# Performance work log

Measured on AMD Instinct MI355X. Metric: run time of the kernel, lower is better.

## Reference

```python
import jax, jax.numpy as jnp
import numpy as np

D_MODEL = 1024
NUM_HEADS = 16


def setup_inputs() -> dict:
    key = jax.random.key(0)
    k1, k2, k3, k4, k5 = jax.random.split(key, 5)
    b, n, d = 4, 2048, D_MODEL
    s = 1.0 / np.sqrt(d)
    x = jax.random.normal(k1, (b, n, d), dtype=jnp.float32)
    v_w = jax.random.uniform(k2, (d, d), dtype=jnp.float32, minval=-s, maxval=s)  # Linear weight [out,in]
    v_b = jax.random.uniform(k3, (d,), dtype=jnp.float32, minval=-s, maxval=s)
    o_w = jax.random.uniform(k4, (d, d), dtype=jnp.float32, minval=-s, maxval=s)
    o_b = jax.random.uniform(k5, (d,), dtype=jnp.float32, minval=-s, maxval=s)
    return {"x": x, "v_w": v_w, "v_b": v_b, "o_w": o_w, "o_b": o_b}


def reference(x, v_w, v_b, o_w, o_b):
    b, n, d = x.shape
    h = NUM_HEADS
    dh = d // h
    # shared QKV projection: q = k = v
    v = jnp.einsum('bnd,ed->bne', x, v_w) + v_b            # [b,n,d]
    v = v.reshape(b, n, h, dh).transpose(0, 2, 1, 3)        # [b,h,n,dh]
    scale = 1.0 / jnp.sqrt(jnp.asarray(dh, dtype=x.dtype))
    scores = jnp.einsum('bhnd,bhmd->bhnm', v, v) * scale    # [b,h,n,n]
    attn = jax.nn.softmax(scores, axis=-1)
    out = jnp.einsum('bhnm,bhmd->bhnd', attn, v)            # [b,h,n,dh]
    out = out.transpose(0, 2, 1, 3).reshape(b, n, d)        # concat heads
    return jnp.einsum('bnd,ed->bne', out, o_w) + o_b
```

## Files before the change

### kernel.cpp

```cpp
#include <hip/hip_runtime.h>
#include <stdint.h>

typedef __attribute__((ext_vector_type(8))) short short8;
typedef __attribute__((ext_vector_type(4))) float f32x4;
typedef __attribute__((ext_vector_type(4))) unsigned int u32x4;
typedef __attribute__((ext_vector_type(2))) unsigned int u32x2;

#define MFMA16(a, b, c) __builtin_amdgcn_mfma_f32_16x16x32_bf16((a), (b), (c), 0, 0, 0)

#define GLD_LDS16(g, l)                                                                  \
    __builtin_amdgcn_global_load_lds((const __attribute__((address_space(1))) void*)(g), \
                                     (__attribute__((address_space(3))) void*)(l), 16, 0, 0)

#if defined(__has_builtin)
#if __has_builtin(__builtin_amdgcn_exp2f)
#define FAST_EXP2(x) __builtin_amdgcn_exp2f(x)
#endif
#endif
#ifndef FAST_EXP2
__device__ __forceinline__ float fast_exp2_asm(float x) {
    float r;
    asm volatile("v_exp_f32 %0, %1\ns_nop 1" : "=v"(r) : "v"(x));
    return r;
}
#define FAST_EXP2(x) fast_exp2_asm(x)
#endif

__device__ __forceinline__ float bf2f(unsigned short u) {
    unsigned int x = ((unsigned int)u) << 16;
    float f;
    __builtin_memcpy(&f, &x, 4);
    return f;
}
__device__ __forceinline__ unsigned short f2bf(float f) {
    unsigned int x;
    __builtin_memcpy(&x, &f, 4);
    unsigned int r = x + 0x7FFFu + ((x >> 16) & 1u);
    return (unsigned short)(r >> 16);
}
__device__ __forceinline__ unsigned int pack2bf(float a, float b) {
    unsigned int ua, ub;
    __builtin_memcpy(&ua, &a, 4);
    __builtin_memcpy(&ub, &b, 4);
    return __builtin_amdgcn_perm(ub + 0x8000u, ua + 0x8000u, 0x07060302u);
}
__device__ __forceinline__ u32x4 cvt8(const float* p) {
    f32x4 g0 = *(const f32x4*)p;
    f32x4 g1 = *(const f32x4*)(p + 4);
    u32x4 r;
    r.x = pack2bf(g0[0], g0[1]);
    r.y = pack2bf(g0[2], g0[3]);
    r.z = pack2bf(g1[0], g1[1]);
    r.w = pack2bf(g1[2], g1[3]);
    return r;
}

__global__ __launch_bounds__(256) void cvt_kernel(const float* __restrict__ in,
                                                  unsigned short* __restrict__ out, int n8) {
    int i = blockIdx.x * 256 + threadIdx.x;
    if (i < n8) *(u32x4*)(out + (size_t)i * 8) = cvt8(in + (size_t)i * 8);
}

template <int MODE>
__global__ __launch_bounds__(256) void gemm_dma_kernel(
    const unsigned short* __restrict__ A, const unsigned short* __restrict__ B,
    const float* __restrict__ bias, void* __restrict__ Cv, int M, int N, int K) {
    __shared__ __align__(16) unsigned short As[2][2][128 * 32];
    __shared__ __align__(16) unsigned short Bs[2][2][128 * 32];

    const int tid = threadIdx.x;
    const int wave = tid >> 6, lane = tid & 63;
    const int l15 = lane & 15, quad = lane >> 4;
    const int m0 = blockIdx.x * 128, n0 = blockIdx.y * 128;
    const int wm = (wave >> 1) * 64, wn = (wave & 1) * 64;

    const int row0 = tid >> 2, c0 = (tid & 3) * 8;
    const unsigned short* Ag0 = A + (size_t)(m0 + row0) * K + c0;
    const unsigned short* Ag1 = A + (size_t)(m0 + row0 + 64) * K + c0;
    const unsigned short* Bg0 = B + (size_t)(n0 + row0) * K + c0;
    const unsigned short* Bg1 = B + (size_t)(n0 + row0 + 64) * K + c0;
    const int wl = wave * 512;

#define STAGE(s, k0)                                     \
    do {                                                 \
        GLD_LDS16(Ag0 + (k0), &As[s][0][wl]);            \
        GLD_LDS16(Ag1 + (k0), &As[s][0][2048 + wl]);     \
        GLD_LDS16(Ag0 + (k0) + 32, &As[s][1][wl]);       \
        GLD_LDS16(Ag1 + (k0) + 32, &As[s][1][2048 + wl]); \
        GLD_LDS16(Bg0 + (k0), &Bs[s][0][wl]);            \
        GLD_LDS16(Bg1 + (k0), &Bs[s][0][2048 + wl]);     \
        GLD_LDS16(Bg0 + (k0) + 32, &Bs[s][1][wl]);       \
        GLD_LDS16(Bg1 + (k0) + 32, &Bs[s][1][2048 + wl]); \
    } while (0)

    f32x4 acc[4][4];
#pragma unroll
    for (int i = 0; i < 4; i++)
#pragma unroll
        for (int j = 0; j < 4; j++) {
            f32x4 z = {0.f, 0.f, 0.f, 0.f};
            acc[i][j] = z;
        }

    STAGE(0, 0);
    for (int k0 = 0; k0 < K; k0 += 64) {
        const int s = (k0 >> 6) & 1;
        __syncthreads();
        if (k0 + 64 < K) STAGE(s ^ 1, k0 + 64);

        short8 a0[4], a1[4], b0[4], b1[4];
#pragma unroll
        for (int mt = 0; mt < 4; mt++) {
            a0[mt] = *(const short8*)&As[s][0][(wm + mt * 16 + l15) * 32 + quad * 8];
            a1[mt] = *(const short8*)&As[s][1][(wm + mt * 16 + l15) * 32 + quad * 8];
        }
#pragma unroll
        for (int nt = 0; nt < 4; nt++) {
            b0[nt] = *(const short8*)&Bs[s][0][(wn + nt * 16 + l15) * 32 + quad * 8];
            b1[nt] = *(const short8*)&Bs[s][1][(wn + nt * 16 + l15) * 32 + quad * 8];
        }
#pragma unroll
        for (int mt = 0; mt < 4; mt++)
#pragma unroll
            for (int nt = 0; nt < 4; nt++) acc[mt][nt] = MFMA16(a0[mt], b0[nt], acc[mt][nt]);
#pragma unroll
        for (int mt = 0; mt < 4; mt++)
#pragma unroll
            for (int nt = 0; nt < 4; nt++) acc[mt][nt] = MFMA16(a1[mt], b1[nt], acc[mt][nt]);
    }
#undef STAGE

    float bv[4];
#pragma unroll
    for (int nt = 0; nt < 4; nt++) bv[nt] = bias[n0 + wn + nt * 16 + l15];

#pragma unroll
    for (int mt = 0; mt < 4; mt++)
#pragma unroll
        for (int nt = 0; nt < 4; nt++)
#pragma unroll
            for (int i = 0; i < 4; i++) {
                int m = m0 + wm + mt * 16 + quad * 4 + i;
                int n = n0 + wn + nt * 16 + l15;
                float val = acc[mt][nt][i] + bv[nt];
                if (MODE == 0) {
                    int bb = m >> 11, ns = m & 2047, h = n >> 6, c = n & 63;
                    ((unsigned short*)Cv)[(size_t)(bb * 16 + h) * 131072 + (size_t)ns * 64 + c] =
                        f2bf(val);
                } else {
                    ((float*)Cv)[(size_t)m * N + n] = val;
                }
            }
}

template <bool AF32, bool BF32, int MODE>
__global__ __launch_bounds__(256) void gemm_bias_kernel(
    const void* __restrict__ Av, const void* __restrict__ Bv,
    const float* __restrict__ bias, void* __restrict__ Cv, int M, int N, int K) {
    __shared__ __align__(16) unsigned short As[128][40];
    __shared__ __align__(16) unsigned short Bs[128][40];

    const int tid = threadIdx.x;
    const int wave = tid >> 6, lane = tid & 63;
    const int l15 = lane & 15, quad = lane >> 4;
    const int m0 = blockIdx.x * 128, n0 = blockIdx.y * 128;
    const int wm = (wave >> 1) * 64, wn = (wave & 1) * 64;

    f32x4 acc[4][4];
#pragma unroll
    for (int i = 0; i < 4; i++)
#pragma unroll
        for (int j = 0; j < 4; j++) {
            f32x4 z = {0.f, 0.f, 0.f, 0.f};
            acc[i][j] = z;
        }

    for (int k0 = 0; k0 < K; k0 += 32) {
        __syncthreads();
#pragma unroll
        for (int rep = 0; rep < 2; rep++) {
            int chunk = tid + rep * 256;
            int row = chunk >> 2, c8 = (chunk & 3) * 8;
            if (AF32) {
                const float* Af = (const float*)Av;
                *(u32x4*)&As[row][c8] = cvt8(&Af[(size_t)(m0 + row) * K + k0 + c8]);
            } else {
                const unsigned short* Ab = (const unsigned short*)Av;
                *(f32x4*)&As[row][c8] = *(const f32x4*)&Ab[(size_t)(m0 + row) * K + k0 + c8];
            }
            if (BF32) {
                const float* Bf = (const float*)Bv;
                *(u32x4*)&Bs[row][c8] = cvt8(&Bf[(size_t)(n0 + row) * K + k0 + c8]);
            } else {
                const unsigned short* Bb = (const unsigned short*)Bv;
                *(f32x4*)&Bs[row][c8] = *(const f32x4*)&Bb[(size_t)(n0 + row) * K + k0 + c8];
            }
        }
        __syncthreads();

        short8 a[4], b[4];
#pragma unroll
        for (int mt = 0; mt < 4; mt++) a[mt] = *(const short8*)&As[wm + mt * 16 + l15][quad * 8];
#pragma unroll
        for (int nt = 0; nt < 4; nt++) b[nt] = *(const short8*)&Bs[wn + nt * 16 + l15][quad * 8];
#pragma unroll
        for (int mt = 0; mt < 4; mt++)
#pragma unroll
            for (int nt = 0; nt < 4; nt++) acc[mt][nt] = MFMA16(a[mt], b[nt], acc[mt][nt]);
    }

    float bv[4];
#pragma unroll
    for (int nt = 0; nt < 4; nt++) bv[nt] = bias[n0 + wn + nt * 16 + l15];

#pragma unroll
    for (int mt = 0; mt < 4; mt++)
#pragma unroll
        for (int nt = 0; nt < 4; nt++)
#pragma unroll
            for (int i = 0; i < 4; i++) {
                int m = m0 + wm + mt * 16 + quad * 4 + i;
                int n = n0 + wn + nt * 16 + l15;
                float val = acc[mt][nt][i] + bv[nt];
                if (MODE == 0) {
                    int bb = m >> 11, ns = m & 2047, h = n >> 6, c = n & 63;
                    ((unsigned short*)Cv)[(size_t)(bb * 16 + h) * 131072 + (size_t)ns * 64 + c] =
                        f2bf(val);
                } else {
                    ((float*)Cv)[(size_t)m * N + n] = val;
                }
            }
}

__global__ __launch_bounds__(256) void transpose_kernel(const unsigned short* __restrict__ V,
                                                        unsigned short* __restrict__ Vt) {
    __shared__ __align__(16) unsigned short T[64][72];
    const int tid = threadIdx.x;
    const int n0 = blockIdx.x * 64;
    const size_t base = (size_t)blockIdx.y * 131072;
#pragma unroll
    for (int rep = 0; rep < 2; rep++) {
        int chunk = tid + rep * 256;
        int row = chunk >> 3, c8 = (chunk & 7) * 8;
        *(short8*)&T[row][c8] = *(const short8*)&V[base + (size_t)(n0 + row) * 64 + c8];
    }
    __syncthreads();
#pragma unroll
    for (int rep = 0; rep < 2; rep++) {
        int chunk = tid + rep * 256;
        int d = chunk >> 3, n8 = (chunk & 7) * 8;
        short8 o;
#pragma unroll
        for (int j = 0; j < 8; j++) o[j] = (short)T[n8 + j][d];
        *(short8*)&Vt[base + (size_t)d * 2048 + n0 + n8] = o;
    }
}

__global__ __launch_bounds__(256, 4) void attn_kernel(const unsigned short* __restrict__ V,
                                                      const unsigned short* __restrict__ Vt,
                                                      unsigned short* __restrict__ O) {
    __shared__ __align__(16) unsigned short QP[128 * 72];
    __shared__ __align__(16) unsigned short Ks0[64 * 32];
    __shared__ __align__(16) unsigned short Ks1[64 * 32];
    __shared__ __align__(16) unsigned short VT0[64 * 32];
    __shared__ __align__(16) unsigned short VT1[64 * 32];

    const int tid = threadIdx.x;
    const int wave = tid >> 6, lane = tid & 63;
    const int l15 = lane & 15, quad = lane >> 4;
    const int q0 = blockIdx.x * 128, bh = blockIdx.y;
    const unsigned short* Vh = V + (size_t)bh * 131072;
    const unsigned short* VhT = Vt + (size_t)bh * 131072;
    const int wm = wave * 32;

#pragma unroll
    for (int rep = 0; rep < 4; rep++) {
        int chunk = tid + rep * 256;
        int row = chunk >> 3, c8 = (chunk & 7) * 8;
        short8 g = *(const short8*)&Vh[(size_t)(q0 + row) * 64 + c8];
        short8 o;
#pragma unroll
        for (int j = 0; j < 8; j++)
            o[j] = (short)f2bf(bf2f((unsigned short)g[j]) * 0.1803368801f);
        *(short8*)&QP[row * 72 + c8] = o;
    }
    __syncthreads();

    short8 bq[2][2];
#pragma unroll
    for (int mt = 0; mt < 2; mt++)
#pragma unroll
        for (int ks = 0; ks < 2; ks++)
            bq[mt][ks] = *(const short8*)&QP[(wm + mt * 16 + l15) * 72 + ks * 32 + quad * 8];

    const int rl = wave * 16 + (lane >> 2);
    const int cl = (lane & 3) * 8;
    const unsigned short* gK = Vh + (size_t)rl * 64 + cl;
    const unsigned short* gVT = VhT + (size_t)rl * 2048 + cl;
    unsigned short* lK0 = Ks0 + wave * 512;
    unsigned short* lK1 = Ks1 + wave * 512;
    unsigned short* lV0 = VT0 + wave * 512;
    unsigned short* lV1 = VT1 + wave * 512;

    f32x4 oacc[2][4];
#pragma unroll
    for (int mt = 0; mt < 2; mt++)
#pragma unroll
        for (int ct = 0; ct < 4; ct++) {
            f32x4 z = {0.f, 0.f, 0.f, 0.f};
            oacc[mt][ct] = z;
        }
    float lsum[2] = {0.f, 0.f};

    for (int kv0 = 0; kv0 < 2048; kv0 += 64) {
        __syncthreads();
        GLD_LDS16(gK + (size_t)kv0 * 64, lK0);
        GLD_LDS16(gK + (size_t)kv0 * 64 + 32, lK1);
        GLD_LDS16(gVT + kv0, lV0);
        GLD_LDS16(gVT + kv0 + 32, lV1);
        __syncthreads();

        f32x4 st[4][2];
#pragma unroll
        for (int nt = 0; nt < 4; nt++) {
            short8 ak0 = *(const short8*)&Ks0[(nt * 16 + l15) * 32 + quad * 8];
            short8 ak1 = *(const short8*)&Ks1[(nt * 16 + l15) * 32 + quad * 8];
#pragma unroll
            for (int mt = 0; mt < 2; mt++) {
                f32x4 z = {0.f, 0.f, 0.f, 0.f};
                z = MFMA16(ak0, bq[mt][0], z);
                z = MFMA16(ak1, bq[mt][1], z);
                st[nt][mt] = z;
            }
        }

#pragma unroll
        for (int mt = 0; mt < 2; mt++) {
            const int prow = (wm + mt * 16 + l15) * 72;
#pragma unroll
            for (int nt = 0; nt < 4; nt++) {
                f32x4 p;
#pragma unroll
                for (int i = 0; i < 4; i++) p[i] = FAST_EXP2(st[nt][mt][i]);
                lsum[mt] += (p[0] + p[1]) + (p[2] + p[3]);
                u32x2 w;
                w.x = pack2bf(p[0], p[1]);
                w.y = pack2bf(p[2], p[3]);
                *(u32x2*)&QP[prow + nt * 16 + quad * 4] = w;
            }
        }
        asm volatile("s_waitcnt lgkmcnt(0)" ::: "memory");

#pragma unroll
        for (int kt = 0; kt < 2; kt++) {
            const unsigned short* VTk = kt ? VT1 : VT0;
            short8 ap[2];
#pragma unroll
            for (int mt = 0; mt < 2; mt++)
                ap[mt] = *(const short8*)&QP[(wm + mt * 16 + l15) * 72 + kt * 32 + quad * 8];
#pragma unroll
            for (int ct = 0; ct < 4; ct++) {
                short8 bvf = *(const short8*)&VTk[(ct * 16 + l15) * 32 + quad * 8];
#pragma unroll
                for (int mt = 0; mt < 2; mt++) oacc[mt][ct] = MFMA16(ap[mt], bvf, oacc[mt][ct]);
            }
        }
    }

    float inv[2][4];
#pragma unroll
    for (int mt = 0; mt < 2; mt++) {
        float v = lsum[mt];
        v += __shfl_xor(v, 16, 64);
        v += __shfl_xor(v, 32, 64);
        float r = 1.0f / v;
#pragma unroll
        for (int i = 0; i < 4; i++) inv[mt][i] = __shfl(r, quad * 4 + i, 16);
    }

    const int bb = bh >> 4, h = bh & 15;
#pragma unroll
    for (int mt = 0; mt < 2; mt++)
#pragma unroll
        for (int i = 0; i < 4; i++) {
            int m = q0 + wm + mt * 16 + quad * 4 + i;
            size_t rowbase = ((size_t)(bb * 2048 + m)) * 1024 + h * 64;
#pragma unroll
            for (int ct = 0; ct < 4; ct++)
                O[rowbase + ct * 16 + l15] = f2bf(oacc[mt][ct][i] * inv[mt][i]);
        }
}

extern "C" void kernel_launch(void* const* d_in, const int* in_sizes, int n_in, void* d_out,
                              int out_size, void* d_ws, size_t ws_size, hipStream_t stream) {
    (void)in_sizes; (void)n_in; (void)out_size;
    const float* x = (const float*)d_in[0];
    const float* v_w = (const float*)d_in[1];
    const float* v_b = (const float*)d_in[2];
    const float* o_w = (const float*)d_in[3];
    const float* o_b = (const float*)d_in[4];
    float* out = (float*)d_out;

    unsigned short* Vbuf = (unsigned short*)d_out;
    unsigned short* Vtbuf = Vbuf + (size_t)8192 * 1024;
    unsigned short* Obuf = (unsigned short*)d_ws;

    const size_t need =
        ((size_t)8192 * 1024  + (size_t)8192 * 1024  + 2 * (size_t)1024 * 1024) * 2;
    if (ws_size >= need) {
        unsigned short* xbf = Obuf + (size_t)8192 * 1024;
        unsigned short* wv = xbf + (size_t)8192 * 1024;
        unsigned short* wo = wv + (size_t)1024 * 1024;
        cvt_kernel<<<4096, 256, 0, stream>>>(x, xbf, 1048576);
        cvt_kernel<<<512, 256, 0, stream>>>(v_w, wv, 131072);
        cvt_kernel<<<512, 256, 0, stream>>>(o_w, wo, 131072);
        gemm_dma_kernel<0><<<dim3(64, 8), 256, 0, stream>>>(xbf, wv, v_b, Vbuf, 8192, 1024, 1024);
        transpose_kernel<<<dim3(32, 64), 256, 0, stream>>>(Vbuf, Vtbuf);
        attn_kernel<<<dim3(16, 64), 256, 0, stream>>>(Vbuf, Vtbuf, Obuf);
        gemm_dma_kernel<1><<<dim3(64, 8), 256, 0, stream>>>(Obuf, wo, o_b, out, 8192, 1024, 1024);
    } else {
        gemm_bias_kernel<true, true, 0>
            <<<dim3(64, 8), 256, 0, stream>>>(x, v_w, v_b, Vbuf, 8192, 1024, 1024);
        transpose_kernel<<<dim3(32, 64), 256, 0, stream>>>(Vbuf, Vtbuf);
        attn_kernel<<<dim3(16, 64), 256, 0, stream>>>(Vbuf, Vtbuf, Obuf);
        gemm_bias_kernel<false, true, 1>
            <<<dim3(64, 8), 256, 0, stream>>>(Obuf, o_w, o_b, out, 8192, 1024, 1024);
    }
}
```

Measured before the change: 229.3 us.

## Double-buffer K/V tiles, XOR-swizzle LDS, remap block order, add setprio

After: 237.3 us. +3.5%, slower.

```diff
diff --git a/kernel.cpp b/kernel.cpp
--- a/kernel.cpp
+++ b/kernel.cpp
@@ -256,51 +256,62 @@
     }
 }
 
-__global__ __launch_bounds__(256, 4) void attn_kernel(const unsigned short* __restrict__ V,
+__global__ __launch_bounds__(256, 3) void attn_kernel(const unsigned short* __restrict__ V,
                                                       const unsigned short* __restrict__ Vt,
                                                       unsigned short* __restrict__ O) {
-    __shared__ __align__(16) unsigned short QP[128 * 72];
-    __shared__ __align__(16) unsigned short Ks0[64 * 32];
-    __shared__ __align__(16) unsigned short Ks1[64 * 32];
-    __shared__ __align__(16) unsigned short VT0[64 * 32];
-    __shared__ __align__(16) unsigned short VT1[64 * 32];
+    __shared__ __align__(16) unsigned short QP[128 * 64];
+    __shared__ __align__(16) unsigned short Ks[2][64 * 64];
+    __shared__ __align__(16) unsigned short VTs[2][64 * 64];
 
     const int tid = threadIdx.x;
     const int wave = tid >> 6, lane = tid & 63;
     const int l15 = lane & 15, quad = lane >> 4;
-    const int q0 = blockIdx.x * 128, bh = blockIdx.y;
+    const int sx = l15 & 7;
+
+    const int flat = blockIdx.y * 16 + blockIdx.x;
+    const int bh = (flat & 7) * 8 + ((flat >> 3) & 7);
+    const int q0 = (flat >> 6) * 128;
+
     const unsigned short* Vh = V + (size_t)bh * 131072;
     const unsigned short* VhT = Vt + (size_t)bh * 131072;
     const int wm = wave * 32;
 
+    const int srow = wave * 16 + (lane >> 3);
+    const int scol = ((lane & 7) ^ (lane >> 3)) * 8;
+    const unsigned short* gK = Vh + (size_t)srow * 64 + scol;
+    const unsigned short* gVT = VhT + (size_t)srow * 2048 + scol;
+
+#define ASTAGE(s, kv)                                                       \
+    do {                                                                    \
+        GLD_LDS16(gK + (size_t)(kv) * 64, &Ks[s][wave * 1024]);             \
+        GLD_LDS16(gK + (size_t)(kv) * 64 + 512, &Ks[s][wave * 1024 + 512]); \
+        GLD_LDS16(gVT + (kv), &VTs[s][wave * 1024]);                        \
+        GLD_LDS16(gVT + (kv) + 8 * 2048, &VTs[s][wave * 1024 + 512]);       \
+    } while (0)
+
+    ASTAGE(0, 0);
+
 #pragma unroll
     for (int rep = 0; rep < 4; rep++) {
         int chunk = tid + rep * 256;
-        int row = chunk >> 3, c8 = (chunk & 7) * 8;
-        short8 g = *(const short8*)&Vh[(size_t)(q0 + row) * 64 + c8];
+        int row = chunk >> 3, cs = chunk & 7;
+        short8 g = *(const short8*)&Vh[(size_t)(q0 + row) * 64 + cs * 8];
         short8 o;
 #pragma unroll
         for (int j = 0; j < 8; j++)
             o[j] = (short)f2bf(bf2f((unsigned short)g[j]) * 0.1803368801f);
-        *(short8*)&QP[row * 72 + c8] = o;
+        *(short8*)&QP[row * 64 + ((cs ^ (row & 7)) << 3)] = o;
     }
     __syncthreads();
 
     short8 bq[2][2];
 #pragma unroll
-    for (int mt = 0; mt < 2; mt++)
+    for (int mt = 0; mt < 2; mt++) {
+        const int row = wm + mt * 16 + l15;
 #pragma unroll
         for (int ks = 0; ks < 2; ks++)
-            bq[mt][ks] = *(const short8*)&QP[(wm + mt * 16 + l15) * 72 + ks * 32 + quad * 8];
-
-    const int rl = wave * 16 + (lane >> 2);
-    const int cl = (lane & 3) * 8;
-    const unsigned short* gK = Vh + (size_t)rl * 64 + cl;
-    const unsigned short* gVT = VhT + (size_t)rl * 2048 + cl;
-    unsigned short* lK0 = Ks0 + wave * 512;
-    unsigned short* lK1 = Ks1 + wave * 512;
-    unsigned short* lV0 = VT0 + wave * 512;
-    unsigned short* lV1 = VT1 + wave * 512;
+            bq[mt][ks] = *(const short8*)&QP[row * 64 + ((((ks << 2) | quad) ^ sx) << 3)];
+    }
 
     f32x4 oacc[2][4];
 #pragma unroll
@@ -313,18 +324,17 @@
     float lsum[2] = {0.f, 0.f};
 
     for (int kv0 = 0; kv0 < 2048; kv0 += 64) {
+        const int s = (kv0 >> 6) & 1;
         __syncthreads();
-        GLD_LDS16(gK + (size_t)kv0 * 64, lK0);
-        GLD_LDS16(gK + (size_t)kv0 * 64 + 32, lK1);
-        GLD_LDS16(gVT + kv0, lV0);
-        GLD_LDS16(gVT + kv0 + 32, lV1);
-        __syncthreads();
+        if (kv0 + 64 < 2048) ASTAGE(s ^ 1, kv0 + 64);
 
         f32x4 st[4][2];
+        __builtin_amdgcn_s_setprio(1);
 #pragma unroll
         for (int nt = 0; nt < 4; nt++) {
-            short8 ak0 = *(const short8*)&Ks0[(nt * 16 + l15) * 32 + quad * 8];
-            short8 ak1 = *(const short8*)&Ks1[(nt * 16 + l15) * 32 + quad * 8];
+            const int krow = (nt * 16 + l15) * 64;
+            short8 ak0 = *(const short8*)&Ks[s][krow + ((quad ^ sx) << 3)];
+            short8 ak1 = *(const short8*)&Ks[s][krow + (((4 | quad) ^ sx) << 3)];
 #pragma unroll
             for (int mt = 0; mt < 2; mt++) {
                 f32x4 z = {0.f, 0.f, 0.f, 0.f};
@@ -333,10 +343,11 @@
                 st[nt][mt] = z;
             }
         }
+        __builtin_amdgcn_s_setprio(0);
 
 #pragma unroll
         for (int mt = 0; mt < 2; mt++) {
-            const int prow = (wm + mt * 16 + l15) * 72;
+            const int prow = (wm + mt * 16 + l15) * 64;
 #pragma unroll
             for (int nt = 0; nt < 4; nt++) {
                 f32x4 p;
@@ -346,26 +357,32 @@
                 u32x2 w;
                 w.x = pack2bf(p[0], p[1]);
                 w.y = pack2bf(p[2], p[3]);
-                *(u32x2*)&QP[prow + nt * 16 + quad * 4] = w;
+                const int slot = (nt * 2 + (quad >> 1)) ^ sx;
+                *(u32x2*)&QP[prow + slot * 8 + (quad & 1) * 4] = w;
             }
         }
         asm volatile("s_waitcnt lgkmcnt(0)" ::: "memory");
 
+        __builtin_amdgcn_s_setprio(1);
 #pragma unroll
         for (int kt = 0; kt < 2; kt++) {
-            const unsigned short* VTk = kt ? VT1 : VT0;
             short8 ap[2];
 #pragma unroll
-            for (int mt = 0; mt < 2; mt++)
-                ap[mt] = *(const short8*)&QP[(wm + mt * 16 + l15) * 72 + kt * 32 + quad * 8];
+            for (int mt = 0; mt < 2; mt++) {
+                const int row = wm + mt * 16 + l15;
+                ap[mt] = *(const short8*)&QP[row * 64 + ((((kt << 2) | quad) ^ sx) << 3)];
+            }
 #pragma unroll
             for (int ct = 0; ct < 4; ct++) {
-                short8 bvf = *(const short8*)&VTk[(ct * 16 + l15) * 32 + quad * 8];
+                short8 bvf =
+                    *(const short8*)&VTs[s][(ct * 16 + l15) * 64 + ((((kt << 2) | quad) ^ sx) << 3)];
 #pragma unroll
                 for (int mt = 0; mt < 2; mt++) oacc[mt][ct] = MFMA16(ap[mt], bvf, oacc[mt][ct]);
             }
         }
-    }
+        __builtin_amdgcn_s_setprio(0);
+    }
+#undef ASTAGE
 
     float inv[2][4];
 #pragma unroll
```
